# Performance work log

Hardware: AMD Instinct MI355X
Metric: run time of the kernel (lower is better)

Reference implementation:

```python
import jax, jax.numpy as jnp
import numpy as np

N_NODES = 100000
N_EDGES = 1600000
IN_CH, HID1, HID2, HID3, OUT_CH = 128, 64, 64, 256, 64


def gcn_conv(x, W, b, src, dst, n_nodes):
    """PyG GCNConv: linear transform, add self-loops, symmetric-normalized aggregation."""
    h = x @ W  # [N, d_out]
    # degree at target nodes, counting the self-loop (+1)
    deg = jnp.zeros((n_nodes,), dtype=h.dtype).at[dst].add(1.0) + 1.0
    dinv = jax.lax.rsqrt(deg)  # deg >= 1, safe
    norm = dinv[src] * dinv[dst]  # [E]
    # scatter-add normalized messages from src to dst
    agg = jnp.zeros_like(h).at[dst].add(h[src] * norm[:, None])
    # self-loop contribution: norm_ii = dinv[i]^2
    agg = agg + h * (dinv * dinv)[:, None]
    return agg + b


def setup_inputs() -> dict:
    key = jax.random.key(0)
    ks = jax.random.split(key, 8)
    x = jax.random.normal(ks[0], (N_NODES, IN_CH), dtype=jnp.float32)
    edge_index = jax.random.randint(ks[1], (2, N_EDGES), 0, N_NODES, dtype=jnp.int64)
    def glorot(k, fan_in, fan_out):
        s = jnp.sqrt(6.0 / (fan_in + fan_out)).astype(jnp.float32)
        return jax.random.uniform(k, (fan_in, fan_out), jnp.float32, -s, s)
    return {
        "x": x,
        "edge_index": edge_index,
        "W1": glorot(ks[2], IN_CH, HID1), "b1": jnp.zeros((HID1,), jnp.float32),
        "W2": glorot(ks[3], HID1, HID2), "b2": jnp.zeros((HID2,), jnp.float32),
        "W3": glorot(ks[4], HID2, HID3), "b3": jnp.zeros((HID3,), jnp.float32),
        "W4": glorot(ks[5], HID3, OUT_CH), "b4": jnp.zeros((OUT_CH,), jnp.float32),
    }


def reference(x, edge_index, W1, b1, W2, b2, W3, b3, W4, b4):
    src, dst = edge_index[0], edge_index[1]
    n = x.shape[0]
    h = jax.nn.relu(gcn_conv(x, W1, b1, src, dst, n))
    h = jax.nn.relu(gcn_conv(h, W2, b2, src, dst, n))
    h = h @ W3 + b3  # hidden Linear (no activation, per original forward)
    h = h @ W4 + b4  # output Linear
    return jax.nn.log_softmax(h, axis=-1)
```

## Files before the change

kernel.cpp:

```cpp
#include <hip/hip_runtime.h>
#include <hip/hip_bf16.h>
#include <math.h>

#define NNODES 100000
#define NEDGES 1600000
#define NB 782
#define PB 256
#define EPB 6250
#define SCAN_N (NB * PB)
#define CAP 4608
#define HTS 72
#define ANB 64

typedef __bf16 bf16x8 __attribute__((ext_vector_type(8)));
typedef float f32x4 __attribute__((ext_vector_type(4)));
typedef unsigned int u32x4 __attribute__((ext_vector_type(4)));
typedef unsigned short u16x8 __attribute__((ext_vector_type(8)));

static __device__ inline unsigned short f2bf(float f) {
    __hip_bfloat16 h = __float2bfloat16(f);
    return *reinterpret_cast<unsigned short*>(&h);
}


static __device__ inline int packidx64(int k, int ch) {
    int s = k >> 5, r5 = k & 31, q = r5 >> 3, ii = r5 & 7;
    int t = ch >> 4, lo = ch & 15;
    int lane = q * 16 + lo;
    return ((t * 2 + s) * 64 + lane) * 8 + ii;
}

__global__ __launch_bounds__(256) void histprep_kernel(const int* __restrict__ dst,
                                                       int* __restrict__ histg,
                                                       const float* __restrict__ W1,
                                                       const float* __restrict__ W2,
                                                       const float* __restrict__ W3,
                                                       const float* __restrict__ W4,
                                                       const float* __restrict__ b3,
                                                       const float* __restrict__ b4,
                                                       unsigned short* __restrict__ Wp1,
                                                       unsigned short* __restrict__ Wp2,
                                                       unsigned short* __restrict__ Wp34,
                                                       float* __restrict__ b34,
                                                       unsigned short* __restrict__ hp) {
    __shared__ int h[NB];
    int tid = threadIdx.x, blk = blockIdx.x;
    if (blk < PB) {
        for (int b = tid; b < NB; b += 256) h[b] = 0;
        __syncthreads();
        int base = blk * EPB;
        for (int i = base + tid; i < base + EPB; i += 256)
            atomicAdd(&h[dst[i] >> 7], 1);
        __syncthreads();
        for (int b = tid; b < NB; b += 256) histg[b * PB + blk] = h[b];
        return;
    }
    int pb = blk - PB;
    if (pb < 32) {
        int idx = pb * 256 + tid;
        int i = idx & 7, rest = idx >> 3;
        int lane = rest & 63; rest >>= 6;
        int s = rest % 4, t = rest / 4;
        int k = s * 32 + (lane >> 4) * 8 + i;
        int ch = t * 16 + (lane & 15);
        Wp1[idx] = f2bf(W1[k * 64 + ch]);
    } else if (pb < 48) {
        int idx = (pb - 32) * 256 + tid;
        int i = idx & 7, rest = idx >> 3;
        int lane = rest & 63; rest >>= 6;
        int s = rest % 2, t = rest / 2;
        int k = s * 32 + (lane >> 4) * 8 + i;
        int ch = t * 16 + (lane & 15);
        Wp2[idx] = f2bf(W2[k * 64 + ch]);
    } else if (pb == 48) {
        if (tid < 64) hp[(size_t)NNODES * 64 + tid] = 0;
    } else if (pb < 65) {
        int i = (pb - 49) * 4 + (tid >> 6);
        int j = tid & 63;
        float a = 0.f;
        for (int k = 0; k < 256; ++k) a = fmaf(W3[i * 256 + k], W4[k * 64 + j], a);
        Wp34[packidx64(i, j)] = f2bf(a);
    } else {
        if (tid < 64) {
            int j = tid;
            float a = b4[j];
            for (int k = 0; k < 256; ++k) a = fmaf(b3[k], W4[k * 64 + j], a);
            b34[j] = a;
        }
    }
}


__global__ __launch_bounds__(256) void scan1_kernel(const int* __restrict__ cnt,
                                                    int* __restrict__ off,
                                                    int* __restrict__ bsum, int n) {
    __shared__ int tmp[256];
    int tid = threadIdx.x;
    int t4 = blockIdx.x * 1024 + tid * 4;
    int v0 = (t4 + 0 < n) ? cnt[t4 + 0] : 0;
    int v1 = (t4 + 1 < n) ? cnt[t4 + 1] : 0;
    int v2 = (t4 + 2 < n) ? cnt[t4 + 2] : 0;
    int v3 = (t4 + 3 < n) ? cnt[t4 + 3] : 0;
    int ssum = v0 + v1 + v2 + v3;
    tmp[tid] = ssum;
    __syncthreads();
    for (int d = 1; d < 256; d <<= 1) {
        int x = (tid >= d) ? tmp[tid - d] : 0;
        __syncthreads();
        tmp[tid] += x;
        __syncthreads();
    }
    int run = tmp[tid] - ssum;
    if (t4 + 0 < n) off[t4 + 0] = run; run += v0;
    if (t4 + 1 < n) off[t4 + 1] = run; run += v1;
    if (t4 + 2 < n) off[t4 + 2] = run; run += v2;
    if (t4 + 3 < n) off[t4 + 3] = run;
    if (tid == 255) bsum[blockIdx.x] = tmp[255];
}

__global__ __launch_bounds__(256) void scan23t_kernel(const int* __restrict__ part_scan,
                                                      const int* __restrict__ bsum,
                                                      const int* __restrict__ histg,
                                                      int* __restrict__ gbaseT,
                                                      int* __restrict__ cntT, int n, int nb) {
    __shared__ int tmp[256];
    __shared__ int bse[256];
    int tid = threadIdx.x;
    int v = (tid < nb) ? bsum[tid] : 0;
    tmp[tid] = v;
    __syncthreads();
    for (int d = 1; d < 256; d <<= 1) {
        int x = (tid >= d) ? tmp[tid - d] : 0;
        __syncthreads();
        tmp[tid] += x;
        __syncthreads();
    }
    bse[tid] = tmp[tid] - v;
    __syncthreads();
    int i = blockIdx.x * 256 + tid;
    if (i < n) {
        int val = part_scan[i] + bse[i >> 10];
        int b = i >> 8, blk = i & 255;
        gbaseT[blk * NB + b] = val;
        cntT[blk * NB + b] = histg[i];
    }
}


__global__ __launch_bounds__(256) void part_kernel(const int* __restrict__ src,
                                                   const int* __restrict__ dst,
                                                   const int* __restrict__ gbaseT,
                                                   const int* __restrict__ cntT,
                                                   unsigned int* __restrict__ part) {
    __shared__ unsigned int sorted[EPB];
    __shared__ int gaddr[EPB];
    __shared__ int gcol[NB];
    __shared__ int base_l[NB];
    __shared__ int cur[NB];
    __shared__ int tmp[256];
    int tid = threadIdx.x, blk = blockIdx.x;
    for (int b = tid; b < NB; b += 256) {
        gcol[b] = gbaseT[blk * NB + b];
        base_l[b] = cntT[blk * NB + b];
        cur[b] = 0;
    }
    __syncthreads();
    int t4 = tid * 4;
    int v0 = (t4 + 0 < NB) ? base_l[t4 + 0] : 0;
    int v1 = (t4 + 1 < NB) ? base_l[t4 + 1] : 0;
    int v2 = (t4 + 2 < NB) ? base_l[t4 + 2] : 0;
    int v3 = (t4 + 3 < NB) ? base_l[t4 + 3] : 0;
    int ssum = v0 + v1 + v2 + v3;
    tmp[tid] = ssum;
    __syncthreads();
    for (int d = 1; d < 256; d <<= 1) {
        int x = (tid >= d) ? tmp[tid - d] : 0;
        __syncthreads();
        tmp[tid] += x;
        __syncthreads();
    }
    int run = tmp[tid] - ssum;
    if (t4 + 0 < NB) base_l[t4 + 0] = run; run += v0;
    if (t4 + 1 < NB) base_l[t4 + 1] = run; run += v1;
    if (t4 + 2 < NB) base_l[t4 + 2] = run; run += v2;
    if (t4 + 3 < NB) base_l[t4 + 3] = run;
    __syncthreads();
    int base = blk * EPB;
    for (int i = base + tid; i < base + EPB; i += 256) {
        int s = src[i], d = dst[i];
        int bkt = d >> 7;
        int r = atomicAdd(&cur[bkt], 1);
        int pos = base_l[bkt] + r;
        sorted[pos] = ((unsigned int)(d & 127) << 17) | (unsigned int)s;
        gaddr[pos] = gcol[bkt] + r;
    }
    __syncthreads();
    for (int i = tid; i < EPB; i += 256)
        part[gaddr[i]] = sorted[i];
}


__global__ __launch_bounds__(256) void csrgemm_kernel(const unsigned int* __restrict__ part,
                                                      const int* __restrict__ gbaseT,
                                                      const float* __restrict__ x,
                                                      const unsigned short* __restrict__ Wp1,
                                                      int* __restrict__ csr,
                                                      int* __restrict__ cnt_g,
                                                      int* __restrict__ off_g,
                                                      float* __restrict__ dinv_g,
                                                      unsigned short* __restrict__ hp, int n) {
    __shared__ unsigned int stage[CAP];
    __shared__ int hist2[128];
    __shared__ int sc[128];
    __shared__ int excl[128];
    __shared__ int cur2[128];
    __shared__ float sdinv[128];
    int tid = threadIdx.x, b = blockIdx.x;
    int S = gbaseT[b];
    int T = (b == NB - 1) ? NEDGES : gbaseT[b + 1];
    int len = T - S;
    bool fit = (len <= CAP);
    if (tid < 128) { hist2[tid] = 0; cur2[tid] = 0; }
    __syncthreads();
    for (int i = tid; i < len; i += 256) {
        unsigned int p = part[S + i];
        if (fit) stage[i] = p;
        atomicAdd(&hist2[p >> 17], 1);
    }
    __syncthreads();
    if (tid < 128) sc[tid] = hist2[tid];
    __syncthreads();
    for (int d = 1; d < 128; d <<= 1) {
        int x2 = 0;
        if (tid < 128 && tid >= d) x2 = sc[tid - d];
        __syncthreads();
        if (tid < 128) sc[tid] += x2;
        __syncthreads();
    }
    if (tid < 128) {
        int c = hist2[tid];
        int ex = sc[tid] - c;
        excl[tid] = ex;
        float dv = rsqrtf((float)c + 1.0f);
        sdinv[tid] = dv;
        int node = b * 128 + tid;
        if (node < n) {
            cnt_g[node] = c;
            off_g[node] = S + ex;
            dinv_g[node] = dv;
        }
    }
    __syncthreads();
    for (int i = tid; i < len; i += 256) {
        unsigned int p = fit ? stage[i] : part[S + i];
        int dl = p >> 17;
        int s = (int)(p & 0x1FFFFu);
        int r = atomicAdd(&cur2[dl], 1);
        csr[S + excl[dl] + r] = s;
    }
    int wv = tid >> 6, lane = tid & 63;
    int q = lane >> 4, lo = lane & 15;
#pragma unroll
    for (int t2 = 0; t2 < 2; ++t2) {
        int nl0 = wv * 32 + t2 * 16;
        int nodeA = b * 128 + nl0 + lo;
        int na = nodeA < n ? nodeA : 0;
        f32x4 acc[4] = {};
#pragma unroll
        for (int s = 0; s < 4; ++s) {
            const float* xr = x + (size_t)na * 128 + q * 8 + s * 32;
            float4 u = *(const float4*)(xr);
            float4 v = *(const float4*)(xr + 4);
            bf16x8 a;
            a[0] = (__bf16)u.x; a[1] = (__bf16)u.y; a[2] = (__bf16)u.z; a[3] = (__bf16)u.w;
            a[4] = (__bf16)v.x; a[5] = (__bf16)v.y; a[6] = (__bf16)v.z; a[7] = (__bf16)v.w;
#pragma unroll
            for (int t = 0; t < 4; ++t) {
                bf16x8 bfr = *(const bf16x8*)(Wp1 + ((size_t)(t * 4 + s) * 64 + lane) * 8);
                acc[t] = __builtin_amdgcn_mfma_f32_16x16x32_bf16(a, bfr, acc[t], 0, 0, 0);
            }
        }
#pragma unroll
        for (int r = 0; r < 4; ++r) {
            int nl = nl0 + q * 4 + r;
            int node = b * 128 + nl;
            if (node < n) {
                float di = sdinv[nl];
#pragma unroll
                for (int t = 0; t < 4; ++t)
                    hp[(size_t)node * 64 + t * 16 + lo] = f2bf(acc[t][r] * di);
            }
        }
    }
}


template <bool LSM>
__global__ __launch_bounds__(256) void aggfuse_kernel(const unsigned short* __restrict__ hsrc,
                                                      const int* __restrict__ csr,
                                                      const int* __restrict__ off,
                                                      const int* __restrict__ cnt,
                                                      const float* __restrict__ dinv,
                                                      const float* __restrict__ biasA,
                                                      const unsigned short* __restrict__ Wp,
                                                      const float* __restrict__ biasB,
                                                      unsigned short* __restrict__ outb,
                                                      float* __restrict__ outf, int n) {
    __shared__ __align__(16) unsigned short ht[ANB * HTS];
    int tid = threadIdx.x, b = blockIdx.x;
    int g = tid >> 3, cl = tid & 7, c8 = cl * 8;
    float4 bv0 = *(const float4*)(biasA + c8);
    float4 bv1 = *(const float4*)(biasA + c8 + 4);
    float bb[8] = {bv0.x, bv0.y, bv0.z, bv0.w, bv1.x, bv1.y, bv1.z, bv1.w};
#pragma unroll 1
    for (int i = 0; i < 2; ++i) {
        int nl = g * 2 + i;
        int node = b * ANB + nl;
        u16x8 hv;
#pragma unroll
        for (int k = 0; k < 8; ++k) hv[k] = 0;
        if (node < n) {
            int s = off[node];
            int c = cnt[node];
            const int* cp = csr + s;
            float acc0[8];
            float acc1[8] = {};
            bf16x8 sv = *(const bf16x8*)(hsrc + (size_t)node * 64 + c8);
            u32x4 su = __builtin_bit_cast(u32x4, sv);
#pragma unroll
            for (int k = 0; k < 4; ++k) {
                acc0[2 * k]     = __builtin_bit_cast(float, su[k] << 16);
                acc0[2 * k + 1] = __builtin_bit_cast(float, su[k] & 0xFFFF0000u);
            }
            int n0 = 0, n1 = 0;
            if (c > 0) n0 = cp[0];
            if (c > 1) n1 = cp[1];
            int j = 0;
            for (; j + 2 <= c; j += 2) {
                bf16x8 va = *(const bf16x8*)(hsrc + (size_t)n0 * 64 + c8);
                bf16x8 vb = *(const bf16x8*)(hsrc + (size_t)n1 * 64 + c8);
                if (j + 3 < c)      { n0 = cp[j + 2]; n1 = cp[j + 3]; }
                else if (j + 2 < c) { n0 = cp[j + 2]; }
                u32x4 ua = __builtin_bit_cast(u32x4, va);
                u32x4 ub = __builtin_bit_cast(u32x4, vb);
#pragma unroll
                for (int k = 0; k < 4; ++k) {
                    acc0[2 * k]     += __builtin_bit_cast(float, ua[k] << 16);
                    acc0[2 * k + 1] += __builtin_bit_cast(float, ua[k] & 0xFFFF0000u);
                    acc1[2 * k]     += __builtin_bit_cast(float, ub[k] << 16);
                    acc1[2 * k + 1] += __builtin_bit_cast(float, ub[k] & 0xFFFF0000u);
                }
            }
            if (j < c) {
                bf16x8 va = *(const bf16x8*)(hsrc + (size_t)n0 * 64 + c8);
                u32x4 ua = __builtin_bit_cast(u32x4, va);
#pragma unroll
                for (int k = 0; k < 4; ++k) {
                    acc0[2 * k]     += __builtin_bit_cast(float, ua[k] << 16);
                    acc0[2 * k + 1] += __builtin_bit_cast(float, ua[k] & 0xFFFF0000u);
                }
            }
            float di = dinv[node];
#pragma unroll
            for (int k = 0; k < 8; ++k)
                hv[k] = f2bf(fmaxf(fmaf(acc0[k] + acc1[k], di, bb[k]), 0.f));
        }
        *(u16x8*)(&ht[nl * HTS + c8]) = hv;
    }
    __syncthreads();
    int wv = tid >> 6, lane = tid & 63;
    int q = lane >> 4, lo = lane & 15;
    int nl0 = wv * 16;
    f32x4 acc[4] = {};
#pragma unroll
    for (int s = 0; s < 2; ++s) {
        bf16x8 a = *(const bf16x8*)(&ht[(nl0 + lo) * HTS + s * 32 + q * 8]);
#pragma unroll
        for (int t = 0; t < 4; ++t) {
            bf16x8 bfr = *(const bf16x8*)(Wp + ((size_t)(t * 2 + s) * 64 + lane) * 8);
            acc[t] = __builtin_amdgcn_mfma_f32_16x16x32_bf16(a, bfr, acc[t], 0, 0, 0);
        }
    }
    if (!LSM) {
#pragma unroll
        for (int r = 0; r < 4; ++r) {
            int node = b * ANB + nl0 + q * 4 + r;
            if (node < n) {
                float di = dinv[node];
#pragma unroll
                for (int t = 0; t < 4; ++t)
                    outb[(size_t)node * 64 + t * 16 + lo] = f2bf(acc[t][r] * di);
            }
        }
    } else {
#pragma unroll
        for (int r = 0; r < 4; ++r) {
            int node = b * ANB + nl0 + q * 4 + r;
            float v0 = acc[0][r] + biasB[0 * 16 + lo];
            float v1 = acc[1][r] + biasB[1 * 16 + lo];
            float v2 = acc[2][r] + biasB[2 * 16 + lo];
            float v3 = acc[3][r] + biasB[3 * 16 + lo];
            float mx = fmaxf(fmaxf(v0, v1), fmaxf(v2, v3));
            for (int d = 1; d < 16; d <<= 1) mx = fmaxf(mx, __shfl_xor(mx, d));
            float sm = __expf(v0 - mx) + __expf(v1 - mx) + __expf(v2 - mx) + __expf(v3 - mx);
            for (int d = 1; d < 16; d <<= 1) sm += __shfl_xor(sm, d);
            float lse = mx + __logf(sm);
            if (node < n) {
                outf[(size_t)node * 64 + 0 * 16 + lo] = v0 - lse;
                outf[(size_t)node * 64 + 1 * 16 + lo] = v1 - lse;
                outf[(size_t)node * 64 + 2 * 16 + lo] = v2 - lse;
                outf[(size_t)node * 64 + 3 * 16 + lo] = v3 - lse;
            }
        }
    }
}


extern "C" void kernel_launch(void* const* d_in, const int* in_sizes, int n_in,
                              void* d_out, int out_size, void* d_ws, size_t ws_size,
                              hipStream_t stream) {
    const float* x  = (const float*)d_in[0];
    const int*   ei = (const int*)d_in[1];
    const float* W1 = (const float*)d_in[2];
    const float* b1 = (const float*)d_in[3];
    const float* W2 = (const float*)d_in[4];
    const float* b2 = (const float*)d_in[5];
    const float* W3 = (const float*)d_in[6];
    const float* b3 = (const float*)d_in[7];
    const float* W4 = (const float*)d_in[8];
    const float* b4 = (const float*)d_in[9];
    float* outp = (float*)d_out;

    const int N = NNODES;
    const int E = NEDGES;
    const int* srcp = ei;
    const int* dstp = ei + E;

    char* w = (char*)d_ws;
    size_t o = 0;
    auto alloc = [&](size_t bytes) { size_t r = o; o = (o + bytes + 255) & ~(size_t)255; return r; };
    size_t cnt_off   = alloc((size_t)N * 4);
    size_t off_off   = alloc((size_t)N * 4);
    size_t dinv_off  = alloc((size_t)N * 4);
    size_t histg_off = alloc((size_t)SCAN_N * 4);
    size_t gscan_off = alloc((size_t)SCAN_N * 4);
    size_t gbT_off   = alloc((size_t)SCAN_N * 4);
    size_t cntT_off  = alloc((size_t)SCAN_N * 4);
    size_t bs_off    = alloc(256 * 4);
    size_t part_off  = alloc((size_t)E * 4);
    size_t csr_off   = alloc((size_t)E * 4);
    size_t hp_off    = alloc((size_t)(N + 1) * 64 * 2);
    size_t abf_off   = alloc((size_t)N * 64 * 2);
    size_t wp1_off   = alloc(128 * 64 * 2);
    size_t wp2_off   = alloc(64 * 64 * 2);
    size_t wp34_off  = alloc(64 * 64 * 2);
    size_t b34_off   = alloc(64 * 4);

    int*            cnt   = (int*)(w + cnt_off);
    int*            off   = (int*)(w + off_off);
    float*          dinv  = (float*)(w + dinv_off);
    int*            histg = (int*)(w + histg_off);
    int*            gscan = (int*)(w + gscan_off);
    int*            gbT   = (int*)(w + gbT_off);
    int*            cntT  = (int*)(w + cntT_off);
    int*            bs    = (int*)(w + bs_off);
    unsigned int*   part  = (unsigned int*)(w + part_off);
    int*            csr   = (int*)(w + csr_off);
    unsigned short* hp    = (unsigned short*)(w + hp_off);
    unsigned short* abf   = (unsigned short*)(w + abf_off);
    unsigned short* Wp1   = (unsigned short*)(w + wp1_off);
    unsigned short* Wp2   = (unsigned short*)(w + wp2_off);
    unsigned short* Wp34  = (unsigned short*)(w + wp34_off);
    float*          b34   = (float*)(w + b34_off);

    const int sb = (SCAN_N + 1023) / 1024;
    const int s3b = (SCAN_N + 255) / 256;

    histprep_kernel<<<PB + 66, 256, 0, stream>>>(dstp, histg, W1, W2, W3, W4, b3, b4,
                                                 Wp1, Wp2, Wp34, b34, hp);
    scan1_kernel<<<sb, 256, 0, stream>>>(histg, gscan, bs, SCAN_N);
    scan23t_kernel<<<s3b, 256, 0, stream>>>(gscan, bs, histg, gbT, cntT, SCAN_N, sb);
    part_kernel<<<PB, 256, 0, stream>>>(srcp, dstp, gbT, cntT, part);
    csrgemm_kernel<<<NB, 256, 0, stream>>>(part, gbT, x, Wp1, csr, cnt, off, dinv, hp, N);

    const int ab = (N + ANB - 1) / ANB;

    aggfuse_kernel<false><<<ab, 256, 0, stream>>>(hp, csr, off, cnt, dinv, b1, Wp2,
                                                  nullptr, abf, nullptr, N);
    aggfuse_kernel<true><<<ab, 256, 0, stream>>>(abf, csr, off, cnt, dinv, b2, Wp34,
                                                 b34, nullptr, outp, N);
}
```

Baseline: 244.4 us.

## Fold scan transpose into partition and CSR kernels, halve partition blocks, unroll gather

Removes the separate transpose/scan-finish kernel. Partition and CSR-build kernels now recompute the block-sum prefix themselves and read the bucket-major scan directly. The partition kernel uses half as many blocks, each handling twice the edges. It drops the per-edge global-address array and finds each edge's bucket with a binary search, which saves shared memory. The aggregation gather loop is unrolled to four neighbors per iteration for more memory-level parallelism. In exchange, each kernel does redundant scans, partition parallelism drops to 128 blocks, and every scatter write now pays for a binary search.

```diff
diff --git a/kernel.cpp b/kernel.cpp
--- a/kernel.cpp
+++ b/kernel.cpp
@@ -5,9 +5,10 @@
 #define NNODES 100000
 #define NEDGES 1600000
 #define NB 782
-#define PB 256
-#define EPB 6250
+#define PB 128
+#define EPB 12500
 #define SCAN_N (NB * PB)
+#define SB ((SCAN_N + 1023) / 1024)
 #define CAP 4608
 #define HTS 72
 #define ANB 64
@@ -118,16 +119,22 @@
     if (tid == 255) bsum[blockIdx.x] = tmp[255];
 }
 
-__global__ __launch_bounds__(256) void scan23t_kernel(const int* __restrict__ part_scan,
-                                                      const int* __restrict__ bsum,
-                                                      const int* __restrict__ histg,
-                                                      int* __restrict__ gbaseT,
-                                                      int* __restrict__ cntT, int n, int nb) {
+
+__global__ __launch_bounds__(256) void part_kernel(const int* __restrict__ src,
+                                                   const int* __restrict__ dst,
+                                                   const int* __restrict__ histg,
+                                                   const int* __restrict__ gscan,
+                                                   const int* __restrict__ bsum,
+                                                   unsigned int* __restrict__ part) {
+    __shared__ unsigned int sorted[EPB];
+    __shared__ int gcol[NB];
+    __shared__ int base_l[NB + 1];
+    __shared__ int cur[NB];
     __shared__ int tmp[256];
     __shared__ int bse[256];
-    int tid = threadIdx.x;
-    int v = (tid < nb) ? bsum[tid] : 0;
-    tmp[tid] = v;
+    int tid = threadIdx.x, blk = blockIdx.x;
+    int bv = (tid < SB) ? bsum[tid] : 0;
+    tmp[tid] = bv;
     __syncthreads();
     for (int d = 1; d < 256; d <<= 1) {
         int x = (tid >= d) ? tmp[tid - d] : 0;
@@ -135,33 +142,12 @@
         tmp[tid] += x;
         __syncthreads();
     }
-    bse[tid] = tmp[tid] - v;
-    __syncthreads();
-    int i = blockIdx.x * 256 + tid;
-    if (i < n) {
-        int val = part_scan[i] + bse[i >> 10];
-        int b = i >> 8, blk = i & 255;
-        gbaseT[blk * NB + b] = val;
-        cntT[blk * NB + b] = histg[i];
-    }
-}
-
-
-__global__ __launch_bounds__(256) void part_kernel(const int* __restrict__ src,
-                                                   const int* __restrict__ dst,
-                                                   const int* __restrict__ gbaseT,
-                                                   const int* __restrict__ cntT,
-                                                   unsigned int* __restrict__ part) {
-    __shared__ unsigned int sorted[EPB];
-    __shared__ int gaddr[EPB];
-    __shared__ int gcol[NB];
-    __shared__ int base_l[NB];
-    __shared__ int cur[NB];
-    __shared__ int tmp[256];
-    int tid = threadIdx.x, blk = blockIdx.x;
+    bse[tid] = tmp[tid] - bv;
+    __syncthreads();
     for (int b = tid; b < NB; b += 256) {
-        gcol[b] = gbaseT[blk * NB + b];
-        base_l[b] = cntT[blk * NB + b];
+        int i = b * PB + blk;
+        gcol[b] = gscan[i] + bse[i >> 10];
+        base_l[b] = histg[i];
         cur[b] = 0;
     }
     __syncthreads();
@@ -184,24 +170,30 @@
     if (t4 + 1 < NB) base_l[t4 + 1] = run; run += v1;
     if (t4 + 2 < NB) base_l[t4 + 2] = run; run += v2;
     if (t4 + 3 < NB) base_l[t4 + 3] = run;
+    if (tid == 0) base_l[NB] = EPB;
     __syncthreads();
     int base = blk * EPB;
     for (int i = base + tid; i < base + EPB; i += 256) {
         int s = src[i], d = dst[i];
         int bkt = d >> 7;
         int r = atomicAdd(&cur[bkt], 1);
-        int pos = base_l[bkt] + r;
-        sorted[pos] = ((unsigned int)(d & 127) << 17) | (unsigned int)s;
-        gaddr[pos] = gcol[bkt] + r;
-    }
-    __syncthreads();
-    for (int i = tid; i < EPB; i += 256)
-        part[gaddr[i]] = sorted[i];
+        sorted[base_l[bkt] + r] = ((unsigned int)(d & 127) << 17) | (unsigned int)s;
+    }
+    __syncthreads();
+    for (int i = tid; i < EPB; i += 256) {
+        int lo = 0, hi = NB;
+        while (hi - lo > 1) {
+            int mid = (lo + hi) >> 1;
+            if (base_l[mid] <= i) lo = mid; else hi = mid;
+        }
+        part[gcol[lo] + (i - base_l[lo])] = sorted[i];
+    }
 }
 
 
 __global__ __launch_bounds__(256) void csrgemm_kernel(const unsigned int* __restrict__ part,
-                                                      const int* __restrict__ gbaseT,
+                                                      const int* __restrict__ gscan,
+                                                      const int* __restrict__ bsum,
                                                       const float* __restrict__ x,
                                                       const unsigned short* __restrict__ Wp1,
                                                       int* __restrict__ csr,
@@ -215,9 +207,23 @@
     __shared__ int excl[128];
     __shared__ int cur2[128];
     __shared__ float sdinv[128];
+    __shared__ int tmp[256];
+    __shared__ int bse[256];
     int tid = threadIdx.x, b = blockIdx.x;
-    int S = gbaseT[b];
-    int T = (b == NB - 1) ? NEDGES : gbaseT[b + 1];
+    int bv = (tid < SB) ? bsum[tid] : 0;
+    tmp[tid] = bv;
+    __syncthreads();
+    for (int d = 1; d < 256; d <<= 1) {
+        int x2 = (tid >= d) ? tmp[tid - d] : 0;
+        __syncthreads();
+        tmp[tid] += x2;
+        __syncthreads();
+    }
+    bse[tid] = tmp[tid] - bv;
+    __syncthreads();
+    int i0 = b * PB;
+    int S = gscan[i0] + bse[i0 >> 10];
+    int T = (b == NB - 1) ? NEDGES : (gscan[i0 + PB] + bse[(i0 + PB) >> 10]);
     int len = T - S;
     bool fit = (len <= CAP);
     if (tid < 128) { hist2[tid] = 0; cur2[tid] = 0; }
@@ -332,27 +338,35 @@
                 acc0[2 * k]     = __builtin_bit_cast(float, su[k] << 16);
                 acc0[2 * k + 1] = __builtin_bit_cast(float, su[k] & 0xFFFF0000u);
             }
-            int n0 = 0, n1 = 0;
-            if (c > 0) n0 = cp[0];
-            if (c > 1) n1 = cp[1];
+            int n0 = 0, n1 = 0, n2 = 0, n3 = 0;
+            if (c >= 4) { n0 = cp[0]; n1 = cp[1]; n2 = cp[2]; n3 = cp[3]; }
             int j = 0;
-            for (; j + 2 <= c; j += 2) {
+            for (; j + 4 <= c; j += 4) {
                 bf16x8 va = *(const bf16x8*)(hsrc + (size_t)n0 * 64 + c8);
                 bf16x8 vb = *(const bf16x8*)(hsrc + (size_t)n1 * 64 + c8);
-                if (j + 3 < c)      { n0 = cp[j + 2]; n1 = cp[j + 3]; }
-                else if (j + 2 < c) { n0 = cp[j + 2]; }
+                bf16x8 vc = *(const bf16x8*)(hsrc + (size_t)n2 * 64 + c8);
+                bf16x8 vd = *(const bf16x8*)(hsrc + (size_t)n3 * 64 + c8);
+                int jn = j + 4;
+                if (jn + 4 <= c) { n0 = cp[jn]; n1 = cp[jn + 1]; n2 = cp[jn + 2]; n3 = cp[jn + 3]; }
                 u32x4 ua = __builtin_bit_cast(u32x4, va);
                 u32x4 ub = __builtin_bit_cast(u32x4, vb);
+                u32x4 uc = __builtin_bit_cast(u32x4, vc);
+                u32x4 ud = __builtin_bit_cast(u32x4, vd);
 #pragma unroll
                 for (int k = 0; k < 4; ++k) {
                     acc0[2 * k]     += __builtin_bit_cast(float, ua[k] << 16);
                     acc0[2 * k + 1] += __builtin_bit_cast(float, ua[k] & 0xFFFF0000u);
                     acc1[2 * k]     += __builtin_bit_cast(float, ub[k] << 16);
                     acc1[2 * k + 1] += __builtin_bit_cast(float, ub[k] & 0xFFFF0000u);
+                    acc0[2 * k]     += __builtin_bit_cast(float, uc[k] << 16);
+                    acc0[2 * k + 1] += __builtin_bit_cast(float, uc[k] & 0xFFFF0000u);
+                    acc1[2 * k]     += __builtin_bit_cast(float, ud[k] << 16);
+                    acc1[2 * k + 1] += __builtin_bit_cast(float, ud[k] & 0xFFFF0000u);
                 }
             }
-            if (j < c) {
-                bf16x8 va = *(const bf16x8*)(hsrc + (size_t)n0 * 64 + c8);
+            for (; j < c; ++j) {
+                int nt = cp[j];
+                bf16x8 va = *(const bf16x8*)(hsrc + (size_t)nt * 64 + c8);
                 u32x4 ua = __builtin_bit_cast(u32x4, va);
 #pragma unroll
                 for (int k = 0; k < 4; ++k) {
@@ -444,8 +458,6 @@
     size_t dinv_off  = alloc((size_t)N * 4);
     size_t histg_off = alloc((size_t)SCAN_N * 4);
     size_t gscan_off = alloc((size_t)SCAN_N * 4);
-    size_t gbT_off   = alloc((size_t)SCAN_N * 4);
-    size_t cntT_off  = alloc((size_t)SCAN_N * 4);
     size_t bs_off    = alloc(256 * 4);
     size_t part_off  = alloc((size_t)E * 4);
     size_t csr_off   = alloc((size_t)E * 4);
@@ -461,8 +473,6 @@
     float*          dinv  = (float*)(w + dinv_off);
     int*            histg = (int*)(w + histg_off);
     int*            gscan = (int*)(w + gscan_off);
-    int*            gbT   = (int*)(w + gbT_off);
-    int*            cntT  = (int*)(w + cntT_off);
     int*            bs    = (int*)(w + bs_off);
     unsigned int*   part  = (unsigned int*)(w + part_off);
     int*            csr   = (int*)(w + csr_off);
@@ -473,15 +483,11 @@
     unsigned short* Wp34  = (unsigned short*)(w + wp34_off);
     float*          b34   = (float*)(w + b34_off);
 
-    const int sb = (SCAN_N + 1023) / 1024;
-    const int s3b = (SCAN_N + 255) / 256;
-
     histprep_kernel<<<PB + 66, 256, 0, stream>>>(dstp, histg, W1, W2, W3, W4, b3, b4,
                                                  Wp1, Wp2, Wp34, b34, hp);
-    scan1_kernel<<<sb, 256, 0, stream>>>(histg, gscan, bs, SCAN_N);
-    scan23t_kernel<<<s3b, 256, 0, stream>>>(gscan, bs, histg, gbT, cntT, SCAN_N, sb);
-    part_kernel<<<PB, 256, 0, stream>>>(srcp, dstp, gbT, cntT, part);
-    csrgemm_kernel<<<NB, 256, 0, stream>>>(part, gbT, x, Wp1, csr, cnt, off, dinv, hp, N);
+    scan1_kernel<<<SB, 256, 0, stream>>>(histg, gscan, bs, SCAN_N);
+    part_kernel<<<PB, 256, 0, stream>>>(srcp, dstp, histg, gscan, bs, part);
+    csrgemm_kernel<<<NB, 256, 0, stream>>>(part, gscan, bs, x, Wp1, csr, cnt, off, dinv, hp, N);
 
     const int ab = (N + ANB - 1) / ANB;
 
```

Result: slower. 286.1 us (+17.1%).
